# Kernel optimization log

Measured on AMD Instinct MI355X. Metric: run time of the kernel, lower is better.

The kernel has to match this reference:

```python
import jax, jax.numpy as jnp
import numpy as np


def setup_inputs() -> dict:
    key = jax.random.key(0)
    k1, k2, k3 = jax.random.split(key, 3)
    N, E, D_IN, D_OUT = 100000, 3200000, 256, 256
    x = jax.random.normal(k1, (N, D_IN), dtype=jnp.float32)
    W = jax.random.normal(k2, (D_OUT, D_IN), dtype=jnp.float32) * (1.0 / np.sqrt(D_IN))
    edge_index = jax.random.randint(k3, (2, E), 0, N, dtype=jnp.int32)
    return {"x": x, "W": W, "edge_index": edge_index}


def reference(x, W, edge_index):
    N = x.shape[0]
    # add self loops (static shape: E + N edges)
    loops = jnp.arange(N, dtype=edge_index.dtype)
    src = jnp.concatenate([edge_index[0], loops])  # [E+N]
    dst = jnp.concatenate([edge_index[1], loops])  # [E+N]
    # symmetric degree normalization: deg = bincount over source index
    deg = jax.ops.segment_sum(jnp.ones_like(src, dtype=x.dtype), src, num_segments=N)
    deg_rsqrt = jax.lax.rsqrt(deg)
    vals = deg_rsqrt[src] * deg_rsqrt[dst]  # [E+N]
    # dense projection then SpMM: out[i] = sum_e A[src_e=i] * h[dst_e]
    h = x @ W.T  # [N, D_OUT]
    msgs = vals[:, None] * h[dst]  # gather + scale
    out = jax.ops.segment_sum(msgs, src, num_segments=N)  # scatter-add
    return out
```

## Files before the change

### kernel.cpp

```cpp
#include <hip/hip_runtime.h>
#include <hip/hip_bf16.h>
#include <stdint.h>

#define D 256
#define NBUCK 391
#define BSHIFT 8
#define TILE 4096

typedef short short8 __attribute__((ext_vector_type(8)));
typedef float f32x4 __attribute__((ext_vector_type(4)));

__device__ __forceinline__ float bf2f(unsigned short u) {
  return __uint_as_float(((unsigned)u) << 16);
}
__device__ __forceinline__ unsigned short f2bf(float f) {
  unsigned u = __float_as_uint(f);
  unsigned r = u + 0x7FFFu + ((u >> 16) & 1u);
  return (unsigned short)(r >> 16);
}

__global__ void bucket_hist_kernel(const int* __restrict__ src, int* __restrict__ bcount, int E) {
  __shared__ int h[NBUCK];
  for (int i = threadIdx.x; i < NBUCK; i += 256) h[i] = 0;
  __syncthreads();
  int gid = blockIdx.x * 256 + threadIdx.x;
  for (int e = gid; e < E; e += 256 * 256) atomicAdd(&h[src[e] >> BSHIFT], 1);
  __syncthreads();
  for (int i = threadIdx.x; i < NBUCK; i += 256) {
    int c = h[i];
    if (c) atomicAdd(&bcount[i], c);
  }
}

__global__ void bucket_scan_kernel(const int* __restrict__ bcount, int* __restrict__ bbase,
                                   int* __restrict__ gcursor) {
  __shared__ int sc[2][512];
  int tid = threadIdx.x;
  sc[0][tid] = (tid < NBUCK) ? bcount[tid] : 0;
  __syncthreads();
  int d = 0;
  for (int off = 1; off < 512; off <<= 1) {
    int v = sc[d][tid];
    if (tid >= off) v += sc[d][tid - off];
    sc[d ^ 1][tid] = v;
    __syncthreads();
    d ^= 1;
  }
  if (tid < NBUCK) {
    int excl = (tid == 0) ? 0 : sc[d][tid - 1];
    bbase[tid] = excl;
    gcursor[tid] = excl;
  }
}

__launch_bounds__(256)
__global__ void binscatter_kernel(const int* __restrict__ src, const int* __restrict__ dst,
                                  int* __restrict__ gcursor, int* __restrict__ ebuf, int E) {
  __shared__ int hist[NBUCK];
  __shared__ int lstart[512];
  __shared__ int gbase[NBUCK];
  __shared__ int sc[2][512];
  __shared__ int stag[TILE];
  __shared__ unsigned short sbuck[TILE];

  int tid = threadIdx.x;
  int base = blockIdx.x * TILE;
  int tilecount = E - base;
  if (tilecount > TILE) tilecount = TILE;

  for (int i = tid; i < NBUCK; i += 256) hist[i] = 0;
  __syncthreads();

  int esrc[16], edst[16];
#pragma unroll
  for (int k = 0; k < 16; k++) {
    int e = base + k * 256 + tid;
    if (e < E) {
      esrc[k] = src[e];
      edst[k] = dst[e];
      atomicAdd(&hist[esrc[k] >> BSHIFT], 1);
    } else {
      esrc[k] = -1;
      edst[k] = 0;
    }
  }
  __syncthreads();

  for (int i = tid; i < 512; i += 256) sc[0][i] = (i < NBUCK) ? hist[i] : 0;
  __syncthreads();
  int d = 0;
  for (int off = 1; off < 512; off <<= 1) {
    for (int i = tid; i < 512; i += 256) {
      int v = sc[d][i];
      if (i >= off) v += sc[d][i - off];
      sc[d ^ 1][i] = v;
    }
    __syncthreads();
    d ^= 1;
  }
  for (int i = tid; i < 512; i += 256) lstart[i] = (i == 0) ? 0 : sc[d][i - 1];
  __syncthreads();

  for (int b = tid; b < NBUCK; b += 256) {
    int c = hist[b];
    if (c) gbase[b] = atomicAdd(&gcursor[b], c);
  }
  __syncthreads();

  for (int i = tid; i < NBUCK; i += 256) hist[i] = 0;
  __syncthreads();

#pragma unroll
  for (int k = 0; k < 16; k++) {
    if (esrc[k] >= 0) {
      int b = esrc[k] >> BSHIFT;
      int r = atomicAdd(&hist[b], 1);
      int pos = lstart[b] + r;
      stag[pos] = edst[k] | ((esrc[k] & 255) << 20);
      sbuck[pos] = (unsigned short)b;
    }
  }
  __syncthreads();

  for (int s = tid; s < tilecount; s += 256) {
    int b = sbuck[s];
    ebuf[gbase[b] + (s - lstart[b])] = stag[s];
  }
}

__launch_bounds__(256)
__global__ void bucketsort_kernel(const int* __restrict__ ebuf, const int* __restrict__ bbase,
                                  const int* __restrict__ bcount, int* __restrict__ csr,
                                  int* __restrict__ offsets, int* __restrict__ ecount,
                                  float* __restrict__ rnorm, int N) {
  __shared__ int ncnt[256];
  __shared__ int nstart[256];
  __shared__ int sc[2][256];
  int tid = threadIdx.x;
  int b = blockIdx.x;
  int base = bbase[b];
  int cnt = bcount[b];
  int node0 = b << BSHIFT;

  ncnt[tid] = 0;
  __syncthreads();
  for (int s = tid; s < cnt; s += 256) {
    int v = ebuf[base + s];
    atomicAdd(&ncnt[v >> 20], 1);
  }
  __syncthreads();

  int mycnt = ncnt[tid];
  sc[0][tid] = mycnt;
  __syncthreads();
  int d = 0;
  for (int off = 1; off < 256; off <<= 1) {
    int v = sc[d][tid];
    if (tid >= off) v += sc[d][tid - off];
    sc[d ^ 1][tid] = v;
    __syncthreads();
    d ^= 1;
  }
  nstart[tid] = (tid == 0) ? 0 : sc[d][tid - 1];
  __syncthreads();

  int node = node0 + tid;
  if (node < N) {
    offsets[node] = base + nstart[tid];
    ecount[node] = mycnt;
    rnorm[node] = rsqrtf((float)(mycnt + 1));
  }

  ncnt[tid] = 0;
  __syncthreads();
  for (int s = tid; s < cnt; s += 256) {
    int v = ebuf[base + s];
    int nl = v >> 20;
    int r = atomicAdd(&ncnt[nl], 1);
    csr[base + nstart[nl] + r] = v & 0xFFFFF;
  }
}

__global__ void convx_kernel(const float* __restrict__ x, unsigned short* __restrict__ xb,
                             int n, int npad) {
  int i4 = blockIdx.x * 256 + threadIdx.x;
  long long elem = (long long)i4 * 4;
  if (elem >= (long long)npad * D) return;
  int row = (int)(elem / D);
  ushort4 o;
  if (row < n) {
    const float4 v = *(const float4*)&x[elem];
    o.x = f2bf(v.x); o.y = f2bf(v.y); o.z = f2bf(v.z); o.w = f2bf(v.w);
  } else {
    o = make_ushort4(0, 0, 0, 0);
  }
  *(ushort4*)&xb[elem] = o;
}

__global__ void convw_kernel(const float* __restrict__ w, unsigned short* __restrict__ wb) {
  int i4 = blockIdx.x * 256 + threadIdx.x;
  int elem = i4 * 4;
  const float4 v = *(const float4*)&w[elem];
  ushort4 o;
  o.x = f2bf(v.x); o.y = f2bf(v.y); o.z = f2bf(v.z); o.w = f2bf(v.w);
  *(ushort4*)&wb[elem] = o;
}

__launch_bounds__(256)
__global__ void gemm_kernel(const unsigned short* __restrict__ A,
                            const unsigned short* __restrict__ B,
                            unsigned short* __restrict__ Hout,
                            const float* __restrict__ rnorm, int n) {
  __shared__ unsigned short sA[128 * 32];
  __shared__ unsigned short sB[128 * 32];
  int tid = threadIdx.x;
  int wave = tid >> 6, lane = tid & 63;
  int wm = wave >> 1, wn = wave & 1;
  int l16 = lane & 15, quad = lane >> 4;
  int arow0 = blockIdx.x * 128;
  int brow0 = blockIdx.y * 128;

  f32x4 acc[4][4];
  const f32x4 zero = {0.f, 0.f, 0.f, 0.f};
#pragma unroll
  for (int i = 0; i < 4; i++)
#pragma unroll
    for (int j = 0; j < 4; j++) acc[i][j] = zero;

  for (int k0 = 0; k0 < 256; k0 += 32) {
#pragma unroll
    for (int it = 0; it < 2; ++it) {
      int c = it * 256 + tid;
      int row = c >> 2, cc = (c & 3) * 8;
      *(int4*)&sA[c * 8] = *(const int4*)&A[(arow0 + row) * 256 + k0 + cc];
      *(int4*)&sB[c * 8] = *(const int4*)&B[(brow0 + row) * 256 + k0 + cc];
    }
    __syncthreads();
    short8 af[4], bfr[4];
#pragma unroll
    for (int i = 0; i < 4; i++)
      af[i] = *(const short8*)&sA[(wm * 64 + i * 16 + l16) * 32 + quad * 8];
#pragma unroll
    for (int j = 0; j < 4; j++)
      bfr[j] = *(const short8*)&sB[(wn * 64 + j * 16 + l16) * 32 + quad * 8];
#pragma unroll
    for (int i = 0; i < 4; i++)
#pragma unroll
      for (int j = 0; j < 4; j++)
        acc[i][j] = __builtin_amdgcn_mfma_f32_16x16x32_bf16(af[i], bfr[j], acc[i][j], 0, 0, 0);
    __syncthreads();
  }

#pragma unroll
  for (int i = 0; i < 4; i++) {
    int rowb = arow0 + wm * 64 + i * 16 + quad * 4;
#pragma unroll
    for (int r = 0; r < 4; r++) {
      int gr = rowb + r;
      float rn = (gr < n) ? rnorm[gr] : 0.f;
#pragma unroll
      for (int j = 0; j < 4; j++) {
        int col = brow0 + wn * 64 + j * 16 + l16;
        Hout[gr * 256 + col] = f2bf(acc[i][j][r] * rn);
      }
    }
  }
}

__launch_bounds__(256)
__global__ void gather_kernel(const unsigned short* __restrict__ hs,
                              const int* __restrict__ offsets,
                              const int* __restrict__ ecount,
                              const float* __restrict__ rnorm,
                              const int* __restrict__ csr,
                              float* __restrict__ out, int n) {
  int wave = threadIdx.x >> 6, lane = threadIdx.x & 63;
  int node = blockIdx.x * 4 + wave;
  if (node >= n) return;
  int start = offsets[node], cnt = ecount[node];
  float a0 = 0.f, a1 = 0.f, a2 = 0.f, a3 = 0.f;
  for (int base = 0; base < cnt; base += 64) {
    int m = cnt - base;
    if (m > 64) m = 64;
    int idxv = 0;
    if (lane < m) idxv = csr[start + base + lane];
    int t = 0;
    for (; t + 4 <= m; t += 4) {
      int d0 = __shfl(idxv, t);
      int d1 = __shfl(idxv, t + 1);
      int d2 = __shfl(idxv, t + 2);
      int d3 = __shfl(idxv, t + 3);
      ushort4 u0 = *(const ushort4*)&hs[d0 * 256 + lane * 4];
      ushort4 u1 = *(const ushort4*)&hs[d1 * 256 + lane * 4];
      ushort4 u2 = *(const ushort4*)&hs[d2 * 256 + lane * 4];
      ushort4 u3 = *(const ushort4*)&hs[d3 * 256 + lane * 4];
      a0 += bf2f(u0.x) + bf2f(u1.x) + bf2f(u2.x) + bf2f(u3.x);
      a1 += bf2f(u0.y) + bf2f(u1.y) + bf2f(u2.y) + bf2f(u3.y);
      a2 += bf2f(u0.z) + bf2f(u1.z) + bf2f(u2.z) + bf2f(u3.z);
      a3 += bf2f(u0.w) + bf2f(u1.w) + bf2f(u2.w) + bf2f(u3.w);
    }
    for (; t < m; ++t) {
      int dd = __shfl(idxv, t);
      ushort4 u = *(const ushort4*)&hs[dd * 256 + lane * 4];
      a0 += bf2f(u.x); a1 += bf2f(u.y); a2 += bf2f(u.z); a3 += bf2f(u.w);
    }
  }
  ushort4 us = *(const ushort4*)&hs[node * 256 + lane * 4];
  float rn = rnorm[node];
  float4 o;
  o.x = rn * (a0 + bf2f(us.x));
  o.y = rn * (a1 + bf2f(us.y));
  o.z = rn * (a2 + bf2f(us.z));
  o.w = rn * (a3 + bf2f(us.w));
  *(float4*)&out[node * 256 + lane * 4] = o;
}

extern "C" void kernel_launch(void* const* d_in, const int* in_sizes, int n_in,
                              void* d_out, int out_size, void* d_ws, size_t ws_size,
                              hipStream_t stream) {
  const float* x = (const float*)d_in[0];
  const float* W = (const float*)d_in[1];
  const int* ei = (const int*)d_in[2];
  float* out = (float*)d_out;

  int N = in_sizes[0] / D;
  int E = in_sizes[2] / 2;
  int NPAD = (N + 127) & ~127;
  const int* src = ei;
  const int* dst = ei + E;

  char* p = (char*)d_ws;
  auto alloc = [&](size_t b) {
    char* r = p;
    p += (b + 255) & ~(size_t)255;
    return r;
  };
  unsigned short* xb = (unsigned short*)alloc((size_t)NPAD * D * 2);
  unsigned short* wb = (unsigned short*)alloc((size_t)D * D * 2);
  unsigned short* hb = (unsigned short*)alloc((size_t)NPAD * D * 2);
  int* csr = (int*)alloc((size_t)E * 4);
  int* offsets = (int*)alloc((size_t)N * 4);
  int* ecount = (int*)alloc((size_t)N * 4);
  float* rnorm = (float*)alloc((size_t)N * 4);
  int* bcount = (int*)alloc(NBUCK * 4);
  int* bbase = (int*)alloc(NBUCK * 4);
  int* gcursor = (int*)alloc(NBUCK * 4);
  int* ebuf = (int*)hb;

  hipMemsetAsync(bcount, 0, NBUCK * 4, stream);
  bucket_hist_kernel<<<256, 256, 0, stream>>>(src, bcount, E);
  bucket_scan_kernel<<<1, 512, 0, stream>>>(bcount, bbase, gcursor);
  binscatter_kernel<<<(E + TILE - 1) / TILE, 256, 0, stream>>>(src, dst, gcursor, ebuf, E);
  bucketsort_kernel<<<NBUCK, 256, 0, stream>>>(ebuf, bbase, bcount, csr, offsets, ecount, rnorm, N);
  convx_kernel<<<(NPAD * (D / 4) + 255) / 256, 256, 0, stream>>>(x, xb, N, NPAD);
  convw_kernel<<<(D * D / 4) / 256, 256, 0, stream>>>(W, wb);
  gemm_kernel<<<dim3(NPAD / 128, D / 128), 256, 0, stream>>>(xb, wb, hb, rnorm, N);
  gather_kernel<<<(N + 3) / 4, 256, 0, stream>>>(hb, offsets, ecount, rnorm, csr, out, N);
}
```

Measured before the change: 539.3 us.

## Fuse bf16 conversion into GEMM, split gather by column halves, widen sort blocks

The GEMM now loads fp32 x and W directly and converts to bf16 while staging into LDS, which removes the separate conversion kernels and their bf16 intermediate buffers. The gather is split into two launches that each handle 128 columns, with half-waves processing alternate edges and a final cross-half reduction, so the gathered working set per pass is smaller and more cache-friendly. The histogram grid and the bucketsort block size are also enlarged to raise parallelism in preprocessing. The costs are redundant W conversion in every GEMM block, a second pass over the CSR indices, and idle threads during the bucketsort scan.

```diff
diff --git a/kernel.cpp b/kernel.cpp
--- a/kernel.cpp
+++ b/kernel.cpp
@@ -24,7 +24,7 @@
   for (int i = threadIdx.x; i < NBUCK; i += 256) h[i] = 0;
   __syncthreads();
   int gid = blockIdx.x * 256 + threadIdx.x;
-  for (int e = gid; e < E; e += 256 * 256) atomicAdd(&h[src[e] >> BSHIFT], 1);
+  for (int e = gid; e < E; e += 1024 * 256) atomicAdd(&h[src[e] >> BSHIFT], 1);
   __syncthreads();
   for (int i = threadIdx.x; i < NBUCK; i += 256) {
     int c = h[i];
@@ -128,7 +128,7 @@
   }
 }
 
-__launch_bounds__(256)
+__launch_bounds__(1024)
 __global__ void bucketsort_kernel(const int* __restrict__ ebuf, const int* __restrict__ bbase,
                                   const int* __restrict__ bcount, int* __restrict__ csr,
                                   int* __restrict__ offsets, int* __restrict__ ecount,
@@ -142,38 +142,42 @@
   int cnt = bcount[b];
   int node0 = b << BSHIFT;
 
-  ncnt[tid] = 0;
-  __syncthreads();
-  for (int s = tid; s < cnt; s += 256) {
+  if (tid < 256) ncnt[tid] = 0;
+  __syncthreads();
+  for (int s = tid; s < cnt; s += 1024) {
     int v = ebuf[base + s];
     atomicAdd(&ncnt[v >> 20], 1);
   }
   __syncthreads();
 
-  int mycnt = ncnt[tid];
-  sc[0][tid] = mycnt;
+  int mycnt = (tid < 256) ? ncnt[tid] : 0;
+  if (tid < 256) sc[0][tid] = mycnt;
   __syncthreads();
   int d = 0;
   for (int off = 1; off < 256; off <<= 1) {
-    int v = sc[d][tid];
-    if (tid >= off) v += sc[d][tid - off];
-    sc[d ^ 1][tid] = v;
+    if (tid < 256) {
+      int v = sc[d][tid];
+      if (tid >= off) v += sc[d][tid - off];
+      sc[d ^ 1][tid] = v;
+    }
     __syncthreads();
     d ^= 1;
   }
-  nstart[tid] = (tid == 0) ? 0 : sc[d][tid - 1];
+  if (tid < 256) {
+    nstart[tid] = (tid == 0) ? 0 : sc[d][tid - 1];
+  }
   __syncthreads();
 
   int node = node0 + tid;
-  if (node < N) {
+  if (tid < 256 && node < N) {
     offsets[node] = base + nstart[tid];
     ecount[node] = mycnt;
     rnorm[node] = rsqrtf((float)(mycnt + 1));
   }
 
-  ncnt[tid] = 0;
-  __syncthreads();
-  for (int s = tid; s < cnt; s += 256) {
+  if (tid < 256) ncnt[tid] = 0;
+  __syncthreads();
+  for (int s = tid; s < cnt; s += 1024) {
     int v = ebuf[base + s];
     int nl = v >> 20;
     int r = atomicAdd(&ncnt[nl], 1);
@@ -181,44 +185,19 @@
   }
 }
 
-__global__ void convx_kernel(const float* __restrict__ x, unsigned short* __restrict__ xb,
-                             int n, int npad) {
-  int i4 = blockIdx.x * 256 + threadIdx.x;
-  long long elem = (long long)i4 * 4;
-  if (elem >= (long long)npad * D) return;
-  int row = (int)(elem / D);
-  ushort4 o;
-  if (row < n) {
-    const float4 v = *(const float4*)&x[elem];
-    o.x = f2bf(v.x); o.y = f2bf(v.y); o.z = f2bf(v.z); o.w = f2bf(v.w);
-  } else {
-    o = make_ushort4(0, 0, 0, 0);
-  }
-  *(ushort4*)&xb[elem] = o;
-}
-
-__global__ void convw_kernel(const float* __restrict__ w, unsigned short* __restrict__ wb) {
-  int i4 = blockIdx.x * 256 + threadIdx.x;
-  int elem = i4 * 4;
-  const float4 v = *(const float4*)&w[elem];
-  ushort4 o;
-  o.x = f2bf(v.x); o.y = f2bf(v.y); o.z = f2bf(v.z); o.w = f2bf(v.w);
-  *(ushort4*)&wb[elem] = o;
-}
-
 __launch_bounds__(256)
-__global__ void gemm_kernel(const unsigned short* __restrict__ A,
-                            const unsigned short* __restrict__ B,
+__global__ void gemm_kernel(const float* __restrict__ X,
+                            const float* __restrict__ W,
                             unsigned short* __restrict__ Hout,
                             const float* __restrict__ rnorm, int n) {
-  __shared__ unsigned short sA[128 * 32];
-  __shared__ unsigned short sB[128 * 32];
+  __shared__ unsigned short sB[16 * 128 * 8];
+  __shared__ unsigned short sA[4 * 128 * 8];
   int tid = threadIdx.x;
   int wave = tid >> 6, lane = tid & 63;
   int wm = wave >> 1, wn = wave & 1;
   int l16 = lane & 15, quad = lane >> 4;
   int arow0 = blockIdx.x * 128;
-  int brow0 = blockIdx.y * 128;
+  int bcol0 = blockIdx.y * 128;
 
   f32x4 acc[4][4];
   const f32x4 zero = {0.f, 0.f, 0.f, 0.f};
@@ -227,28 +206,48 @@
 #pragma unroll
     for (int j = 0; j < 4; j++) acc[i][j] = zero;
 
-  for (int k0 = 0; k0 < 256; k0 += 32) {
-#pragma unroll
-    for (int it = 0; it < 2; ++it) {
-      int c = it * 256 + tid;
-      int row = c >> 2, cc = (c & 3) * 8;
-      *(int4*)&sA[c * 8] = *(const int4*)&A[(arow0 + row) * 256 + k0 + cc];
-      *(int4*)&sB[c * 8] = *(const int4*)&B[(brow0 + row) * 256 + k0 + cc];
-    }
-    __syncthreads();
-    short8 af[4], bfr[4];
-#pragma unroll
-    for (int i = 0; i < 4; i++)
-      af[i] = *(const short8*)&sA[(wm * 64 + i * 16 + l16) * 32 + quad * 8];
-#pragma unroll
-    for (int j = 0; j < 4; j++)
-      bfr[j] = *(const short8*)&sB[(wn * 64 + j * 16 + l16) * 32 + quad * 8];
-#pragma unroll
-    for (int i = 0; i < 4; i++)
+  for (int khalf = 0; khalf < 2; khalf++) {
+    int kbase = khalf * 128;
+#pragma unroll
+    for (int it = 0; it < 16; ++it) {
+      int i = it * 256 + tid;
+      int col = i >> 5;
+      int kk = (i & 31) * 4;
+      const float4 v = *(const float4*)&W[(bcol0 + col) * 256 + kbase + kk];
+      ushort4 o;
+      o.x = f2bf(v.x); o.y = f2bf(v.y); o.z = f2bf(v.z); o.w = f2bf(v.w);
+      *(ushort4*)&sB[(kk >> 3) * 1024 + col * 8 + (kk & 7)] = o;
+    }
+    for (int k0 = kbase; k0 < kbase + 128; k0 += 32) {
+#pragma unroll
+      for (int it = 0; it < 4; ++it) {
+        int i = it * 256 + tid;
+        int row = i >> 3;
+        int kk = (i & 7) * 4;
+        int gr = arow0 + row;
+        float4 v;
+        if (gr < n) v = *(const float4*)&X[(size_t)gr * 256 + k0 + kk];
+        else { v.x = v.y = v.z = v.w = 0.f; }
+        ushort4 o;
+        o.x = f2bf(v.x); o.y = f2bf(v.y); o.z = f2bf(v.z); o.w = f2bf(v.w);
+        *(ushort4*)&sA[(kk >> 3) * 1024 + row * 8 + (kk & 7)] = o;
+      }
+      __syncthreads();
+      int kc = (k0 - kbase) >> 3;
+      short8 af[4], bfr[4];
+#pragma unroll
+      for (int i = 0; i < 4; i++)
+        af[i] = *(const short8*)&sA[quad * 1024 + (wm * 64 + i * 16 + l16) * 8];
 #pragma unroll
       for (int j = 0; j < 4; j++)
-        acc[i][j] = __builtin_amdgcn_mfma_f32_16x16x32_bf16(af[i], bfr[j], acc[i][j], 0, 0, 0);
-    __syncthreads();
+        bfr[j] = *(const short8*)&sB[(kc + quad) * 1024 + (wn * 64 + j * 16 + l16) * 8];
+#pragma unroll
+      for (int i = 0; i < 4; i++)
+#pragma unroll
+        for (int j = 0; j < 4; j++)
+          acc[i][j] = __builtin_amdgcn_mfma_f32_16x16x32_bf16(af[i], bfr[j], acc[i][j], 0, 0, 0);
+      __syncthreads();
+    }
   }
 
 #pragma unroll
@@ -260,7 +259,7 @@
       float rn = (gr < n) ? rnorm[gr] : 0.f;
 #pragma unroll
       for (int j = 0; j < 4; j++) {
-        int col = brow0 + wn * 64 + j * 16 + l16;
+        int col = bcol0 + wn * 64 + j * 16 + l16;
         Hout[gr * 256 + col] = f2bf(acc[i][j][r] * rn);
       }
     }
@@ -273,11 +272,13 @@
                               const int* __restrict__ ecount,
                               const float* __restrict__ rnorm,
                               const int* __restrict__ csr,
-                              float* __restrict__ out, int n) {
+                              float* __restrict__ out, int n, int colbase) {
   int wave = threadIdx.x >> 6, lane = threadIdx.x & 63;
+  int h = lane >> 5, li = lane & 31;
   int node = blockIdx.x * 4 + wave;
   if (node >= n) return;
   int start = offsets[node], cnt = ecount[node];
+  const unsigned short* hcol = hs + colbase + li * 4;
   float a0 = 0.f, a1 = 0.f, a2 = 0.f, a3 = 0.f;
   for (int base = 0; base < cnt; base += 64) {
     int m = cnt - base;
@@ -285,34 +286,49 @@
     int idxv = 0;
     if (lane < m) idxv = csr[start + base + lane];
     int t = 0;
-    for (; t + 4 <= m; t += 4) {
-      int d0 = __shfl(idxv, t);
-      int d1 = __shfl(idxv, t + 1);
-      int d2 = __shfl(idxv, t + 2);
-      int d3 = __shfl(idxv, t + 3);
-      ushort4 u0 = *(const ushort4*)&hs[d0 * 256 + lane * 4];
-      ushort4 u1 = *(const ushort4*)&hs[d1 * 256 + lane * 4];
-      ushort4 u2 = *(const ushort4*)&hs[d2 * 256 + lane * 4];
-      ushort4 u3 = *(const ushort4*)&hs[d3 * 256 + lane * 4];
-      a0 += bf2f(u0.x) + bf2f(u1.x) + bf2f(u2.x) + bf2f(u3.x);
-      a1 += bf2f(u0.y) + bf2f(u1.y) + bf2f(u2.y) + bf2f(u3.y);
-      a2 += bf2f(u0.z) + bf2f(u1.z) + bf2f(u2.z) + bf2f(u3.z);
-      a3 += bf2f(u0.w) + bf2f(u1.w) + bf2f(u2.w) + bf2f(u3.w);
-    }
-    for (; t < m; ++t) {
-      int dd = __shfl(idxv, t);
-      ushort4 u = *(const ushort4*)&hs[dd * 256 + lane * 4];
-      a0 += bf2f(u.x); a1 += bf2f(u.y); a2 += bf2f(u.z); a3 += bf2f(u.w);
-    }
-  }
-  ushort4 us = *(const ushort4*)&hs[node * 256 + lane * 4];
-  float rn = rnorm[node];
-  float4 o;
-  o.x = rn * (a0 + bf2f(us.x));
-  o.y = rn * (a1 + bf2f(us.y));
-  o.z = rn * (a2 + bf2f(us.z));
-  o.w = rn * (a3 + bf2f(us.w));
-  *(float4*)&out[node * 256 + lane * 4] = o;
+    for (; t + 8 <= m; t += 8) {
+      int e0 = __shfl(idxv, t + h);
+      int e1 = __shfl(idxv, t + 2 + h);
+      int e2 = __shfl(idxv, t + 4 + h);
+      int e3 = __shfl(idxv, t + 6 + h);
+      uint2 u0 = *(const uint2*)&hcol[e0 * 256];
+      uint2 u1 = *(const uint2*)&hcol[e1 * 256];
+      uint2 u2 = *(const uint2*)&hcol[e2 * 256];
+      uint2 u3 = *(const uint2*)&hcol[e3 * 256];
+      a0 += bf2f((unsigned short)u0.x) + bf2f((unsigned short)u1.x) +
+            bf2f((unsigned short)u2.x) + bf2f((unsigned short)u3.x);
+      a1 += bf2f((unsigned short)(u0.x >> 16)) + bf2f((unsigned short)(u1.x >> 16)) +
+            bf2f((unsigned short)(u2.x >> 16)) + bf2f((unsigned short)(u3.x >> 16));
+      a2 += bf2f((unsigned short)u0.y) + bf2f((unsigned short)u1.y) +
+            bf2f((unsigned short)u2.y) + bf2f((unsigned short)u3.y);
+      a3 += bf2f((unsigned short)(u0.y >> 16)) + bf2f((unsigned short)(u1.y >> 16)) +
+            bf2f((unsigned short)(u2.y >> 16)) + bf2f((unsigned short)(u3.y >> 16));
+    }
+    for (; t < m; t += 2) {
+      int dd = __shfl(idxv, t + h);
+      if (t + h < m) {
+        uint2 u = *(const uint2*)&hcol[dd * 256];
+        a0 += bf2f((unsigned short)u.x);
+        a1 += bf2f((unsigned short)(u.x >> 16));
+        a2 += bf2f((unsigned short)u.y);
+        a3 += bf2f((unsigned short)(u.y >> 16));
+      }
+    }
+  }
+  a0 += __shfl_xor(a0, 32);
+  a1 += __shfl_xor(a1, 32);
+  a2 += __shfl_xor(a2, 32);
+  a3 += __shfl_xor(a3, 32);
+  if (h == 0) {
+    uint2 us = *(const uint2*)&hcol[node * 256];
+    float rn = rnorm[node];
+    float4 o;
+    o.x = rn * (a0 + bf2f((unsigned short)us.x));
+    o.y = rn * (a1 + bf2f((unsigned short)(us.x >> 16)));
+    o.z = rn * (a2 + bf2f((unsigned short)us.y));
+    o.w = rn * (a3 + bf2f((unsigned short)(us.y >> 16)));
+    *(float4*)&out[node * 256 + colbase + li * 4] = o;
+  }
 }
 
 extern "C" void kernel_launch(void* const* d_in, const int* in_sizes, int n_in,
@@ -335,8 +351,6 @@
     p += (b + 255) & ~(size_t)255;
     return r;
   };
-  unsigned short* xb = (unsigned short*)alloc((size_t)NPAD * D * 2);
-  unsigned short* wb = (unsigned short*)alloc((size_t)D * D * 2);
   unsigned short* hb = (unsigned short*)alloc((size_t)NPAD * D * 2);
   int* csr = (int*)alloc((size_t)E * 4);
   int* offsets = (int*)alloc((size_t)N * 4);
@@ -348,12 +362,11 @@
   int* ebuf = (int*)hb;
 
   hipMemsetAsync(bcount, 0, NBUCK * 4, stream);
-  bucket_hist_kernel<<<256, 256, 0, stream>>>(src, bcount, E);
+  bucket_hist_kernel<<<1024, 256, 0, stream>>>(src, bcount, E);
   bucket_scan_kernel<<<1, 512, 0, stream>>>(bcount, bbase, gcursor);
   binscatter_kernel<<<(E + TILE - 1) / TILE, 256, 0, stream>>>(src, dst, gcursor, ebuf, E);
-  bucketsort_kernel<<<NBUCK, 256, 0, stream>>>(ebuf, bbase, bcount, csr, offsets, ecount, rnorm, N);
-  convx_kernel<<<(NPAD * (D / 4) + 255) / 256, 256, 0, stream>>>(x, xb, N, NPAD);
-  convw_kernel<<<(D * D / 4) / 256, 256, 0, stream>>>(W, wb);
-  gemm_kernel<<<dim3(NPAD / 128, D / 128), 256, 0, stream>>>(xb, wb, hb, rnorm, N);
-  gather_kernel<<<(N + 3) / 4, 256, 0, stream>>>(hb, offsets, ecount, rnorm, csr, out, N);
-}
+  bucketsort_kernel<<<NBUCK, 1024, 0, stream>>>(ebuf, bbase, bcount, csr, offsets, ecount, rnorm, N);
+  gemm_kernel<<<dim3(NPAD / 128, D / 128), 256, 0, stream>>>(x, W, hb, rnorm, N);
+  gather_kernel<<<(N + 3) / 4, 256, 0, stream>>>(hb, offsets, ecount, rnorm, csr, out, N, 0);
+  gather_kernel<<<(N + 3) / 4, 256, 0, stream>>>(hb, offsets, ecount, rnorm, csr, out, N, 128);
+}
```

Result: slower. 552.7 us (+2.5%).
